# Performance work log

Measured on AMD Instinct MI355X. Metric: run time of the kernel, lower is better.

The kernel has to match this reference:

```python
import jax, jax.numpy as jnp
import numpy as np

N = 2_097_152   # flattened batch (rows of the ODE state)
D = 64          # feature dim; odefunc must map R^D -> R^D
T = 1.0         # integration_time; rk4 over grid [0, T] = one step of size h=T


def setup_inputs() -> dict:
    key = jax.random.key(0)
    kx, k1, k2 = jax.random.split(key, 3)
    scale = 1.0 / np.sqrt(D)
    return {
        "x": jax.random.normal(kx, (N, D), dtype=jnp.float32),
        "W1": jax.random.normal(k1, (D, D), dtype=jnp.float32) * scale,
        "b1": jnp.zeros((D,), dtype=jnp.float32),
        "W2": jax.random.normal(k2, (D, D), dtype=jnp.float32) * scale,
        "b2": jnp.zeros((D,), dtype=jnp.float32),
    }


def reference(x, W1, b1, W2, b2):
    # odefunc f(t, y): autonomous 2-layer tanh MLP (t unused)
    def f(y):
        return jnp.tanh(y @ W1 + b1) @ W2 + b2

    # torchdiffeq rk4 on grid [0, T] -> single classic RK4 step, h = T
    h = jnp.float32(T)
    k1 = f(x)
    k2 = f(x + 0.5 * h * k1)
    k3 = f(x + 0.5 * h * k2)
    k4 = f(x + h * k3)
    # out = odeint(...)[1]
    return x + (h / 6.0) * (k1 + 2.0 * k2 + 2.0 * k3 + k4)
```

## Files before the change

### kernel.cpp

```cpp
#include <hip/hip_runtime.h>

typedef __attribute__((ext_vector_type(8))) short short8;
typedef __attribute__((ext_vector_type(16))) float f32x16;

union FragU { unsigned u[4]; short8 s8; };

__device__ __forceinline__ unsigned cvt_pk_bf16(float lo, float hi) {
  unsigned r;
  asm("v_cvt_pk_bf16_f32 %0, %1, %2" : "=v"(r) : "v"(lo), "v"(hi));
  return r;
}
__device__ __forceinline__ void perm32_swap(unsigned& a, unsigned& b) {
  asm volatile("v_permlane32_swap_b32 %0, %1" : "+v"(a), "+v"(b));
}
__device__ __forceinline__ float bf_lo(unsigned u) { return __uint_as_float(u << 16); }
__device__ __forceinline__ float bf_hi(unsigned u) { return __uint_as_float(u & 0xffff0000u); }
__device__ __forceinline__ unsigned short f2bf(float f) {
  union { float f; unsigned u; } v; v.f = f;
  unsigned r = v.u + 0x7FFFu + ((v.u >> 16) & 1u);
  return (unsigned short)(r >> 16);
}
__device__ __forceinline__ float tanh_fast(float x) {
  float e = __expf(2.0f * x);
  float r = __builtin_amdgcn_rcpf(e + 1.0f);
  return 1.0f - 2.0f * r;
}
__device__ __forceinline__ f32x16 zero16() {
  f32x16 z;
  #pragma unroll
  for (int i = 0; i < 16; ++i) z[i] = 0.0f;
  return z;
}

__device__ __forceinline__ void build_frags(unsigned p[16], FragU F[4]) {
  #pragma unroll
  for (int kt = 0; kt < 4; ++kt) {
    perm32_swap(p[4*kt+0], p[4*kt+2]);
    perm32_swap(p[4*kt+1], p[4*kt+3]);
    F[kt].u[0] = p[4*kt+0]; F[kt].u[1] = p[4*kt+1];
    F[kt].u[2] = p[4*kt+2]; F[kt].u[3] = p[4*kt+3];
  }
}

__device__ __forceinline__ void matmul(const short8 wa[4][2], const short8 bA[2],
                                       const short8 ones, const FragU F[4],
                                       f32x16& c0, f32x16& c1) {
  f32x16 z = zero16();
  c0 = __builtin_amdgcn_mfma_f32_32x32x16_bf16(bA[0], ones, z, 0, 0, 0);
  c1 = __builtin_amdgcn_mfma_f32_32x32x16_bf16(bA[1], ones, z, 0, 0, 0);
  #pragma unroll
  for (int kt = 0; kt < 4; ++kt) {
    c0 = __builtin_amdgcn_mfma_f32_32x32x16_bf16(wa[kt][0], F[kt].s8, c0, 0, 0, 0);
    c1 = __builtin_amdgcn_mfma_f32_32x32x16_bf16(wa[kt][1], F[kt].s8, c1, 0, 0, 0);
  }
}

__device__ __forceinline__ void tanh_pack(unsigned p[16], const f32x16& c0, const f32x16& c1) {
  #pragma unroll
  for (int g = 0; g < 8; ++g) {
    const f32x16& c = (g < 4) ? c0 : c1;
    int rg = g & 3;
    p[2*g+0] = cvt_pk_bf16(tanh_fast(c[4*rg+0]), tanh_fast(c[4*rg+1]));
    p[2*g+1] = cvt_pk_bf16(tanh_fast(c[4*rg+2]), tanh_fast(c[4*rg+3]));
  }
}

__device__ __forceinline__ void ypack(unsigned p[16], const unsigned xb[16], float cc,
                                      const f32x16& k0, const f32x16& k1) {
  #pragma unroll
  for (int g = 0; g < 8; ++g) {
    const f32x16& k = (g < 4) ? k0 : k1;
    int rg = g & 3;
    float y0 = bf_lo(xb[2*g+0]) + cc * k[4*rg+0];
    float y1 = bf_hi(xb[2*g+0]) + cc * k[4*rg+1];
    float y2 = bf_lo(xb[2*g+1]) + cc * k[4*rg+2];
    float y3 = bf_hi(xb[2*g+1]) + cc * k[4*rg+3];
    p[2*g+0] = cvt_pk_bf16(y0, y1);
    p[2*g+1] = cvt_pk_bf16(y2, y3);
  }
}

__global__ __launch_bounds__(256, 2)
void ode_rk4_kernel(const float* __restrict__ x, const float* __restrict__ W1,
                    const float* __restrict__ b1, const float* __restrict__ W2,
                    const float* __restrict__ b2, float* __restrict__ out,
                    int nstrips)
{
  const int tid  = threadIdx.x;
  const int lane = tid & 63;
  const int ln   = lane & 31;
  const int hl   = lane >> 5;
  const int wv   = tid >> 6;

  short8 w1a[4][2], w2a[4][2];
  #pragma unroll
  for (int kt = 0; kt < 4; ++kt)
    #pragma unroll
    for (int mt = 0; mt < 2; ++mt) {
      int c = ln + 32*mt, kb = 16*kt + 8*hl;
      FragU f1, f2;
      #pragma unroll
      for (int j = 0; j < 4; ++j) {
        f1.u[j] = cvt_pk_bf16(W1[(kb+2*j)*64 + c], W1[(kb+2*j+1)*64 + c]);
        f2.u[j] = cvt_pk_bf16(W2[(kb+2*j)*64 + c], W2[(kb+2*j+1)*64 + c]);
      }
      w1a[kt][mt] = f1.s8; w2a[kt][mt] = f2.s8;
    }

  FragU onesF; onesF.u[0] = hl ? 0u : 0x3F80u; onesF.u[1] = onesF.u[2] = onesF.u[3] = 0u;
  short8 b1A[2], b2A[2];
  #pragma unroll
  for (int mt = 0; mt < 2; ++mt) {
    FragU fb1, fb2;
    fb1.u[0] = hl ? 0u : (unsigned)f2bf(b1[ln + 32*mt]);
    fb2.u[0] = hl ? 0u : (unsigned)f2bf(b2[ln + 32*mt]);
    fb1.u[1] = fb1.u[2] = fb1.u[3] = 0u;
    fb2.u[1] = fb2.u[2] = fb2.u[3] = 0u;
    b1A[mt] = fb1.s8; b2A[mt] = fb2.s8;
  }

  const int gw  = gridDim.x * 4;
  int wid       = blockIdx.x * 4 + wv;
  const int lnoff = ln * 16 + hl;

  for (int s = wid; s < nstrips; s += gw) {
    const float4* xs4 = (const float4*)x   + (size_t)s * 512;
    float4*       os4 = (float4*)out       + (size_t)s * 512;

    unsigned xb[16];
    #pragma unroll
    for (int g = 0; g < 8; ++g) {
      float4 v = xs4[lnoff + 8*(g>>2) + 2*(g&3)];
      xb[2*g+0] = cvt_pk_bf16(v.x, v.y);
      xb[2*g+1] = cvt_pk_bf16(v.z, v.w);
    }

    f32x16 acc0, acc1, ct0, ct1;
    FragU F[4];
    unsigned p[16];

    #pragma unroll
    for (int i = 0; i < 16; ++i) p[i] = xb[i];
    build_frags(p, F);
    matmul(w1a, b1A, onesF.s8, F, ct0, ct1);
    tanh_pack(p, ct0, ct1);
    build_frags(p, F);
    matmul(w2a, b2A, onesF.s8, F, ct0, ct1);
    acc0 = ct0; acc1 = ct1;

    #pragma unroll
    for (int st = 1; st < 4; ++st) {
      const float cc = (st == 3) ? 1.0f : 0.5f;
      const float wc = (st == 3) ? 1.0f : 2.0f;
      ypack(p, xb, cc, ct0, ct1);
      build_frags(p, F);
      matmul(w1a, b1A, onesF.s8, F, ct0, ct1);
      tanh_pack(p, ct0, ct1);
      build_frags(p, F);
      matmul(w2a, b2A, onesF.s8, F, ct0, ct1);
      acc0 += wc * ct0; acc1 += wc * ct1;
    }

    #pragma unroll
    for (int g = 0; g < 8; ++g) {
      const f32x16& a = (g < 4) ? acc0 : acc1;
      int rg = g & 3;
      float4 o;
      o.x = bf_lo(xb[2*g+0]) + (1.0f/6.0f) * a[4*rg+0];
      o.y = bf_hi(xb[2*g+0]) + (1.0f/6.0f) * a[4*rg+1];
      o.z = bf_lo(xb[2*g+1]) + (1.0f/6.0f) * a[4*rg+2];
      o.w = bf_hi(xb[2*g+1]) + (1.0f/6.0f) * a[4*rg+3];
      os4[lnoff + 8*(g>>2) + 2*(g&3)] = o;
    }
  }
}

extern "C" void kernel_launch(void* const* d_in, const int* in_sizes, int n_in,
                              void* d_out, int out_size, void* d_ws, size_t ws_size,
                              hipStream_t stream) {
  const float* x  = (const float*)d_in[0];
  const float* W1 = (const float*)d_in[1];
  const float* b1 = (const float*)d_in[2];
  const float* W2 = (const float*)d_in[3];
  const float* b2 = (const float*)d_in[4];
  float* out = (float*)d_out;
  int nstrips = in_sizes[0] / 2048;
  ode_rk4_kernel<<<1024, 256, 0, stream>>>(x, W1, b1, W2, b2, out, nstrips);
}
```

Before: 1.089 ms.

## Move bf16 weight fragments from registers to LDS to raise occupancy

```diff
diff --git a/kernel.cpp b/kernel.cpp
--- a/kernel.cpp
+++ b/kernel.cpp
@@ -42,16 +42,18 @@
   }
 }
 
-__device__ __forceinline__ void matmul(const short8 wa[4][2], const short8 bA[2],
-                                       const short8 ones, const FragU F[4],
-                                       f32x16& c0, f32x16& c1) {
-  f32x16 z = zero16();
-  c0 = __builtin_amdgcn_mfma_f32_32x32x16_bf16(bA[0], ones, z, 0, 0, 0);
-  c1 = __builtin_amdgcn_mfma_f32_32x32x16_bf16(bA[1], ones, z, 0, 0, 0);
+__device__ __forceinline__ void matmulL(const short8 (*w)[64], int lane,
+                                        short8 bA0, short8 bA1, short8 ones,
+                                        const f32x16& z, const FragU F[4],
+                                        f32x16& c0, f32x16& c1) {
+  c0 = __builtin_amdgcn_mfma_f32_32x32x16_bf16(bA0, ones, z, 0, 0, 0);
+  c1 = __builtin_amdgcn_mfma_f32_32x32x16_bf16(bA1, ones, z, 0, 0, 0);
   #pragma unroll
   for (int kt = 0; kt < 4; ++kt) {
-    c0 = __builtin_amdgcn_mfma_f32_32x32x16_bf16(wa[kt][0], F[kt].s8, c0, 0, 0, 0);
-    c1 = __builtin_amdgcn_mfma_f32_32x32x16_bf16(wa[kt][1], F[kt].s8, c1, 0, 0, 0);
+    short8 w0 = w[2*kt+0][lane];
+    short8 w1 = w[2*kt+1][lane];
+    c0 = __builtin_amdgcn_mfma_f32_32x32x16_bf16(w0, F[kt].s8, c0, 0, 0, 0);
+    c1 = __builtin_amdgcn_mfma_f32_32x32x16_bf16(w1, F[kt].s8, c1, 0, 0, 0);
   }
 }
 
@@ -80,23 +82,24 @@
   }
 }
 
-__global__ __launch_bounds__(256, 2)
+__global__ __launch_bounds__(256, 3)
 void ode_rk4_kernel(const float* __restrict__ x, const float* __restrict__ W1,
                     const float* __restrict__ b1, const float* __restrict__ W2,
                     const float* __restrict__ b2, float* __restrict__ out,
                     int nstrips)
 {
+  __shared__ short8 wlds[16][64];
+
   const int tid  = threadIdx.x;
   const int lane = tid & 63;
   const int ln   = lane & 31;
   const int hl   = lane >> 5;
   const int wv   = tid >> 6;
 
-  short8 w1a[4][2], w2a[4][2];
-  #pragma unroll
-  for (int kt = 0; kt < 4; ++kt)
+  if (wv == 0) {
     #pragma unroll
-    for (int mt = 0; mt < 2; ++mt) {
+    for (int f = 0; f < 8; ++f) {
+      int kt = f >> 1, mt = f & 1;
       int c = ln + 32*mt, kb = 16*kt + 8*hl;
       FragU f1, f2;
       #pragma unroll
@@ -104,8 +107,10 @@
         f1.u[j] = cvt_pk_bf16(W1[(kb+2*j)*64 + c], W1[(kb+2*j+1)*64 + c]);
         f2.u[j] = cvt_pk_bf16(W2[(kb+2*j)*64 + c], W2[(kb+2*j+1)*64 + c]);
       }
-      w1a[kt][mt] = f1.s8; w2a[kt][mt] = f2.s8;
+      wlds[f    ][lane] = f1.s8;
+      wlds[8 + f][lane] = f2.s8;
     }
+  }
 
   FragU onesF; onesF.u[0] = hl ? 0u : 0x3F80u; onesF.u[1] = onesF.u[2] = onesF.u[3] = 0u;
   short8 b1A[2], b2A[2];
@@ -118,6 +123,9 @@
     fb2.u[1] = fb2.u[2] = fb2.u[3] = 0u;
     b1A[mt] = fb1.s8; b2A[mt] = fb2.s8;
   }
+  const f32x16 z = zero16();
+
+  __syncthreads();
 
   const int gw  = gridDim.x * 4;
   int wid       = blockIdx.x * 4 + wv;
@@ -142,10 +150,10 @@
     #pragma unroll
     for (int i = 0; i < 16; ++i) p[i] = xb[i];
     build_frags(p, F);
-    matmul(w1a, b1A, onesF.s8, F, ct0, ct1);
+    matmulL(&wlds[0], lane, b1A[0], b1A[1], onesF.s8, z, F, ct0, ct1);
     tanh_pack(p, ct0, ct1);
     build_frags(p, F);
-    matmul(w2a, b2A, onesF.s8, F, ct0, ct1);
+    matmulL(&wlds[8], lane, b2A[0], b2A[1], onesF.s8, z, F, ct0, ct1);
     acc0 = ct0; acc1 = ct1;
 
     #pragma unroll
@@ -154,10 +162,10 @@
       const float wc = (st == 3) ? 1.0f : 2.0f;
       ypack(p, xb, cc, ct0, ct1);
       build_frags(p, F);
-      matmul(w1a, b1A, onesF.s8, F, ct0, ct1);
+      matmulL(&wlds[0], lane, b1A[0], b1A[1], onesF.s8, z, F, ct0, ct1);
       tanh_pack(p, ct0, ct1);
       build_frags(p, F);
-      matmul(w2a, b2A, onesF.s8, F, ct0, ct1);
+      matmulL(&wlds[8], lane, b2A[0], b2A[1], onesF.s8, z, F, ct0, ct1);
       acc0 += wc * ct0; acc1 += wc * ct1;
     }
 
@@ -185,5 +193,5 @@
   const float* b2 = (const float*)d_in[4];
   float* out = (float*)d_out;
   int nstrips = in_sizes[0] / 2048;
-  ode_rk4_kernel<<<1024, 256, 0, stream>>>(x, W1, b1, W2, b2, out, nstrips);
+  ode_rk4_kernel<<<768, 256, 0, stream>>>(x, W1, b1, W2, b2, out, nstrips);
 }
```

After: 1.148 ms. 5.4% more time.
